# Optimization experiments

Measured on AMD Instinct MI355X. Metric: run time of the kernel, lower is better.

## Reference

```python
import jax, jax.numpy as jnp
import numpy as np

N, E, IN, H, OUT, G = 50000, 800000, 128, 256, 10, 512


def setup_inputs() -> dict:
    key = jax.random.key(0)
    ks = jax.random.split(key, 12)
    def lin(k, fan_in, fan_out):
        s = 1.0 / np.sqrt(fan_in)
        kw, kb = jax.random.split(k)
        W = jax.random.uniform(kw, (fan_in, fan_out), jnp.float32, -s, s)
        b = jax.random.uniform(kb, (fan_out,), jnp.float32, -s, s)
        return W, b
    x = jax.random.normal(ks[0], (N, IN), jnp.float32)
    edge_index = jax.random.randint(ks[1], (2, E), 0, N)
    batch = jnp.sort(jax.random.randint(ks[2], (N,), 0, G))
    W1a, b1a = lin(ks[3], IN, H)
    W1b, b1b = lin(ks[4], H, H)
    W2a, b2a = lin(ks[5], H, H)
    W2b, b2b = lin(ks[6], H, H)
    Wlin, blin = lin(ks[7], H, OUT)
    eps1 = jnp.zeros((), jnp.float32)
    eps2 = jnp.zeros((), jnp.float32)
    return dict(x=x, edge_index=edge_index, batch=batch,
                eps1=eps1, W1a=W1a, b1a=b1a, W1b=W1b, b1b=b1b,
                eps2=eps2, W2a=W2a, b2a=b2a, W2b=W2b, b2b=b2b,
                Wlin=Wlin, blin=blin)


def reference(x, edge_index, batch, eps1, W1a, b1a, W1b, b1b,
              eps2, W2a, b2a, W2b, b2b, Wlin, blin):
    src, dst = edge_index[0], edge_index[1]
    # GINConv 1: h = MLP((1+eps)*x + sum_{j in N(i)} x_j)
    agg = jax.ops.segment_sum(x[src], dst, num_segments=N)  # [N, IN]
    h = (1.0 + eps1) * x + agg
    h = jax.nn.relu(h @ W1a + b1a) @ W1b + b1b              # [N, H]
    h = jax.nn.relu(h)  # (dropout p=0.3 is identity in eval mode)
    # GINConv 2
    agg2 = jax.ops.segment_sum(h[src], dst, num_segments=N)  # [N, H]
    h2 = (1.0 + eps2) * h + agg2
    h2 = jax.nn.relu(h2 @ W2a + b2a) @ W2b + b2b             # [N, H]
    # global mean pool per graph
    psum = jax.ops.segment_sum(h2, batch, num_segments=G)    # [G, H]
    cnt = jax.ops.segment_sum(jnp.ones((N, 1), h2.dtype), batch, num_segments=G)
    pooled = psum / jnp.maximum(cnt, 1.0)
    out = pooled @ Wlin + blin                               # [G, OUT]
    return jax.nn.log_softmax(out, axis=-1)
```

## Files before the change

kernel.cpp:

```cpp
#include <hip/hip_runtime.h>
#include <math.h>
#include <stdint.h>

constexpr int N   = 50000;
constexpr int E   = 800000;
constexpr int IN  = 128;
constexpr int H   = 256;
constexpr int OUT = 10;
constexpr int G   = 512;
constexpr int BSTR = 64;

constexpr int NPART  = 391;
constexpr int SEGCAP = 48;
constexpr int EPB    = 4096;
constexpr int AB     = (E + EPB - 1) / EPB;

typedef __bf16 bf16x8 __attribute__((ext_vector_type(8)));
typedef float  f32x4  __attribute__((ext_vector_type(4)));
typedef float  f32x2  __attribute__((ext_vector_type(2)));

__device__ __forceinline__ float blo(unsigned v) { return __uint_as_float(v << 16); }
__device__ __forceinline__ float bhi(unsigned v) { return __uint_as_float(v & 0xffff0000u); }
__device__ __forceinline__ unsigned short f2b(float f) {
  unsigned u = __float_as_uint(f);
  u += 0x7fffu + ((u >> 16) & 1u);
  return (unsigned short)(u >> 16);
}
__device__ __forceinline__ unsigned packb(float lo, float hi) {
  return (unsigned)f2b(lo) | ((unsigned)f2b(hi) << 16);
}
__device__ __forceinline__ unsigned pk_fp8x4(float a, float b, float c, float d) {
  int r = 0;
  r = __builtin_amdgcn_cvt_pk_fp8_f32(a, b, r, false);
  r = __builtin_amdgcn_cvt_pk_fp8_f32(c, d, r, true);
  return (unsigned)r;
}
__device__ __forceinline__ unsigned char fp8_1(float v) {
  return (unsigned char)(__builtin_amdgcn_cvt_pk_fp8_f32(v, v, 0, false) & 0xff);
}

__device__ __forceinline__ void acc16(float* a, uint4 w, float s) {
  unsigned ws[4] = {w.x, w.y, w.z, w.w};
#pragma unroll
  for (int d = 0; d < 4; ++d) {
    f32x2 lo = __builtin_amdgcn_cvt_pk_f32_fp8((int)ws[d], false);
    f32x2 hi = __builtin_amdgcn_cvt_pk_f32_fp8((int)ws[d], true);
    a[4*d+0] = fmaf(s, lo.x, a[4*d+0]);
    a[4*d+1] = fmaf(s, lo.y, a[4*d+1]);
    a[4*d+2] = fmaf(s, hi.x, a[4*d+2]);
    a[4*d+3] = fmaf(s, hi.y, a[4*d+3]);
  }
}


constexpr int XQ_BLOCKS  = (N * IN / 4) / 256;
constexpr int W1A_BLOCKS = (256 * IN) / 256;
constexpr int WH_BLOCKS  = (256 * H) / 256;

__global__ __launch_bounds__(256) void prep_kernel(
    const int* __restrict__ srcp, const int* __restrict__ dstp,
    unsigned* __restrict__ pbuf, int* __restrict__ pcnt,
    const float* __restrict__ x, unsigned* __restrict__ xq,
    const float* __restrict__ W1a, unsigned short* __restrict__ Wt1a,
    const float* __restrict__ W1b, unsigned short* __restrict__ Wt1b,
    const float* __restrict__ W2a, unsigned short* __restrict__ Wt2a,
    const float* __restrict__ W2b, unsigned short* __restrict__ Wt2b) {
  __shared__ int lcur[NPART];
  int b = blockIdx.x;
  int t = threadIdx.x;
  if (b < AB) {
    for (int j = t; j < NPART; j += 256) lcur[j] = 0;
    __syncthreads();
    const int e0 = b * EPB;
#pragma unroll
    for (int r = 0; r < EPB / 1024; ++r) {
      int base = e0 + (r * 256 + t) * 4;
      if (base < E) {
        int4 d4 = *(const int4*)(dstp + base);
        int4 s4 = *(const int4*)(srcp + base);
        int dd[4] = {d4.x, d4.y, d4.z, d4.w};
        int ss[4] = {s4.x, s4.y, s4.z, s4.w};
#pragma unroll
        for (int u = 0; u < 4; ++u) {
          int part = dd[u] >> 7, dl = dd[u] & 127;
          int pos = atomicAdd(&lcur[part], 1);
          if (pos < SEGCAP)
            pbuf[((size_t)part * AB + b) * SEGCAP + pos] =
                ((unsigned)dl << 16) | (unsigned)ss[u];
        }
      }
    }
    __syncthreads();
    for (int j = t; j < NPART; j += 256) pcnt[b * NPART + j] = min(lcur[j], SEGCAP);
    return;
  }
  b -= AB;
  if (b < XQ_BLOCKS) {
    int id = b * 256 + t;
    float4 v = ((const float4*)x)[id];
    xq[id] = pk_fp8x4(v.x, v.y, v.z, v.w);
    return;
  }
  b -= XQ_BLOCKS;
  if (b < W1A_BLOCKS) {
    int id = b * 256 + t;
    int n = id >> 7, k = id & 127;
    Wt1a[id] = f2b(W1a[k * 256 + n]);
    return;
  }
  b -= W1A_BLOCKS;
  const float* Ws;
  unsigned short* Wd;
  if (b < WH_BLOCKS)            { Ws = W1b; Wd = Wt1b; }
  else if (b < 2 * WH_BLOCKS)   { Ws = W2a; Wd = Wt2a; b -= WH_BLOCKS; }
  else                          { Ws = W2b; Wd = Wt2b; b -= 2 * WH_BLOCKS; }
  int id = b * 256 + t;
  int n = id >> 8, k = id & 255;
  Wd[id] = f2b(Ws[k * 256 + n]);
}


__global__ __launch_bounds__(256) void csr_kernel(const unsigned* __restrict__ pbuf,
                                                  const int* __restrict__ pcnt,
                                                  int* __restrict__ deg, int* __restrict__ csre) {
  __shared__ int sa[256], sb[256];
  __shared__ int ldeg[128];
  int p = blockIdx.x;
  int t = threadIdx.x;
  if (t < 128) ldeg[t] = 0;
  sa[t] = (t < AB) ? pcnt[t * NPART + p] : 0;
  __syncthreads();
  int* cur = sa; int* nxt = sb;
#pragma unroll
  for (int off = 1; off < 256; off <<= 1) {
    nxt[t] = cur[t] + ((t >= off) ? cur[t - off] : 0);
    __syncthreads();
    int* tmp = cur; cur = nxt; nxt = tmp;
  }
  int T = cur[255];
  const unsigned* seg = pbuf + (size_t)p * AB * SEGCAP;
  for (int f = t; f < T; f += 256) {
    int lo = 0, hi = AB - 1;
    while (lo < hi) { int m = (lo + hi) >> 1; if (cur[m] > f) hi = m; else lo = m + 1; }
    int bb = lo;
    int excl = bb ? cur[bb - 1] : 0;
    unsigned v = seg[(size_t)bb * SEGCAP + (f - excl)];
    int dl = (int)(v >> 16), s = (int)(v & 0xFFFFu);
    int pos = atomicAdd(&ldeg[dl], 1);
    if (pos < BSTR) csre[(((size_t)p << 7) + dl) * BSTR + pos] = s;
  }
  __syncthreads();
  if (t < 128) {
    int node = (p << 7) + t;
    if (node < N) deg[node] = min(ldeg[t], BSTR);
  }
}


template <int K1, bool RELU2, bool OUT8>
__global__ __launch_bounds__(256, 2) void fused_mlp_kernel(
    const unsigned char* __restrict__ inq,
    const int* __restrict__ deg, const int* __restrict__ csre,
    const float* __restrict__ epsp,
    const unsigned short* __restrict__ Bta,
    const float* __restrict__ ba,
    const unsigned short* __restrict__ Btb,
    const float* __restrict__ bb,
    void* __restrict__ outv, int Nrows) {
  constexpr int LDK = 40, LDI = 168;
  constexpr int LDA = K1 + 40;
  constexpr int TPN = K1 / 32;
  constexpr int NPP = 256 / TPN;
  constexpr int PASSES = 64 / NPP;
  __shared__ __align__(16) unsigned short sh[10240 + 64 * LDA];
  unsigned short* Bs = sh;
  unsigned short* Af = sh + 10240;
  unsigned short* Is = sh + 10240;
  const int tid  = threadIdx.x;
  const int r0   = blockIdx.x * 64;
  const int wave = tid >> 6, lane = tid & 63;
  const int quad = lane >> 4, l15 = lane & 15;
  const int wrow = (wave >> 1) * 32, wcol = (wave & 1) * 64;
  const int srow = tid >> 2;
  const int sk8  = (tid & 3) * 8;

  {
    const float sc = 1.0f + epsp[0];
    const int slot = tid % TPN;
    const int nd0  = tid / TPN;
    const unsigned char* rb = inq + slot * 32;
#pragma unroll
    for (int ps = 0; ps < PASSES; ++ps) {
      const int node = ps * NPP + nd0;
      const int i = r0 + node;
      float a[32];
#pragma unroll
      for (int q = 0; q < 32; ++q) a[q] = 0.f;
      if (i < Nrows) {
        int dg = deg[i]; if (dg > BSTR) dg = BSTR;
        const int* bkt = csre + (size_t)i * BSTR;
        int j = 0;
        for (; j + 4 <= dg; j += 4) {
          uint4 v[8];
#pragma unroll
          for (int u = 0; u < 4; ++u) {
            unsigned raw = (unsigned)bkt[j + u];
            if (raw >= (unsigned)N) raw = 0u;
            const uint4* src = (const uint4*)(rb + (size_t)raw * K1);
            v[2*u]   = src[0];
            v[2*u+1] = src[1];
          }
#pragma unroll
          for (int u = 0; u < 4; ++u) {
            acc16(a,      v[2*u],   1.0f);
            acc16(a + 16, v[2*u+1], 1.0f);
          }
        }
        for (; j < dg; ++j) {
          unsigned raw = (unsigned)bkt[j];
          if (raw >= (unsigned)N) raw = 0u;
          const uint4* src = (const uint4*)(rb + (size_t)raw * K1);
          acc16(a, src[0], 1.0f);
          acc16(a + 16, src[1], 1.0f);
        }
        const uint4* sr = (const uint4*)(rb + (size_t)i * K1);
        acc16(a, sr[0], sc);
        acc16(a + 16, sr[1], sc);
      }
      uint4* dst = (uint4*)(Af + node * LDA + slot * 32);
#pragma unroll
      for (int w = 0; w < 4; ++w)
        dst[w] = make_uint4(packb(a[8*w+0], a[8*w+1]), packb(a[8*w+2], a[8*w+3]),
                            packb(a[8*w+4], a[8*w+5]), packb(a[8*w+6], a[8*w+7]));
    }
  }

  f32x4 acc1[2][2][4];
#pragma unroll
  for (int c = 0; c < 2; ++c)
#pragma unroll
    for (int i = 0; i < 2; ++i)
#pragma unroll
      for (int j = 0; j < 4; ++j) acc1[c][i][j] = (f32x4){0.f, 0.f, 0.f, 0.f};

  for (int k0 = 0; k0 < K1; k0 += 32) {
#pragma unroll
    for (int sgm = 0; sgm < 4; ++sgm) {
      int col = srow + sgm * 64;
      *(uint4*)(Bs + col * LDK + sk8) = *(const uint4*)(Bta + (size_t)col * K1 + k0 + sk8);
    }
    __syncthreads();
    bf16x8 af[2];
#pragma unroll
    for (int mt = 0; mt < 2; ++mt)
      af[mt] = *(const bf16x8*)(Af + (wrow + mt * 16 + l15) * LDA + k0 + quad * 8);
#pragma unroll
    for (int ch = 0; ch < 2; ++ch) {
      bf16x8 bfr[4];
#pragma unroll
      for (int nt = 0; nt < 4; ++nt)
        bfr[nt] = *(const bf16x8*)(Bs + (ch * 128 + wcol + nt * 16 + l15) * LDK + quad * 8);
#pragma unroll
      for (int mt = 0; mt < 2; ++mt)
#pragma unroll
        for (int nt = 0; nt < 4; ++nt)
          acc1[ch][mt][nt] =
              __builtin_amdgcn_mfma_f32_16x16x32_bf16(af[mt], bfr[nt], acc1[ch][mt][nt], 0, 0, 0);
    }
    __syncthreads();
  }

  float bva[2][4];
#pragma unroll
  for (int c = 0; c < 2; ++c)
#pragma unroll
    for (int nt = 0; nt < 4; ++nt) bva[c][nt] = ba[c * 128 + wcol + nt * 16 + l15];

  f32x4 acc2[2][2][4];
#pragma unroll
  for (int c = 0; c < 2; ++c)
#pragma unroll
    for (int i = 0; i < 2; ++i)
#pragma unroll
      for (int j = 0; j < 4; ++j) acc2[c][i][j] = (f32x4){0.f, 0.f, 0.f, 0.f};

  for (int ch = 0; ch < 2; ++ch) {
    __syncthreads();
#pragma unroll
    for (int mt = 0; mt < 2; ++mt)
#pragma unroll
      for (int nt = 0; nt < 4; ++nt) {
        int col = wcol + nt * 16 + l15;
        int rbase = wrow + mt * 16 + quad * 4;
#pragma unroll
        for (int i = 0; i < 4; ++i)
          Is[(rbase + i) * LDI + col] = f2b(fmaxf(acc1[ch][mt][nt][i] + bva[ch][nt], 0.f));
      }
    for (int kk = 0; kk < 4; ++kk) {
      __syncthreads();
      {
        int k0 = ch * 128 + kk * 32;
#pragma unroll
        for (int sgm = 0; sgm < 4; ++sgm) {
          int col = srow + sgm * 64;
          *(uint4*)(Bs + col * LDK + sk8) = *(const uint4*)(Btb + (size_t)col * 256 + k0 + sk8);
        }
      }
      __syncthreads();
      bf16x8 af[2];
#pragma unroll
      for (int mt = 0; mt < 2; ++mt)
        af[mt] = *(const bf16x8*)(Is + (wrow + mt * 16 + l15) * LDI + kk * 32 + quad * 8);
#pragma unroll
      for (int c2 = 0; c2 < 2; ++c2) {
        bf16x8 bfr[4];
#pragma unroll
        for (int nt = 0; nt < 4; ++nt)
          bfr[nt] = *(const bf16x8*)(Bs + (c2 * 128 + wcol + nt * 16 + l15) * LDK + quad * 8);
#pragma unroll
        for (int mt = 0; mt < 2; ++mt)
#pragma unroll
          for (int nt = 0; nt < 4; ++nt)
            acc2[c2][mt][nt] =
                __builtin_amdgcn_mfma_f32_16x16x32_bf16(af[mt], bfr[nt], acc2[c2][mt][nt], 0, 0, 0);
      }
    }
    __syncthreads();
  }

#pragma unroll
  for (int c2 = 0; c2 < 2; ++c2) {
    float bv[4];
#pragma unroll
    for (int nt = 0; nt < 4; ++nt) bv[nt] = bb[c2 * 128 + wcol + nt * 16 + l15];
#pragma unroll
    for (int mt = 0; mt < 2; ++mt) {
      int gr0 = r0 + wrow + mt * 16 + quad * 4;
#pragma unroll
      for (int i = 0; i < 4; ++i) {
        int grow = gr0 + i;
        if (grow >= Nrows) continue;
#pragma unroll
        for (int nt = 0; nt < 4; ++nt) {
          float v = acc2[c2][mt][nt][i] + bv[nt];
          if (RELU2) v = fmaxf(v, 0.f);
          int col = c2 * 128 + wcol + nt * 16 + l15;
          if (OUT8) ((unsigned char*)outv)[(size_t)grow * 256 + col] = fp8_1(v);
          else      ((unsigned short*)outv)[(size_t)grow * 256 + col] = f2b(v);
        }
      }
    }
  }
}


__global__ __launch_bounds__(128) void pool_final_kernel(const unsigned short* __restrict__ h2,
                                                         const int* __restrict__ batch,
                                                         const float* __restrict__ Wlin,
                                                         const float* __restrict__ blin,
                                                         float* __restrict__ out) {
  __shared__ float sp[H];
  __shared__ float logits[OUT];
  int g = blockIdx.x;
  int t = threadIdx.x;
  int lo = 0, hi = N;
  while (lo < hi) { int m = (lo + hi) >> 1; if (batch[m] < g) lo = m + 1; else hi = m; }
  int s = lo;
  lo = 0; hi = N;
  while (lo < hi) { int m = (lo + hi) >> 1; if (batch[m] < g + 1) lo = m + 1; else hi = m; }
  int e = lo;
  float a0 = 0.f, a1 = 0.f;
  const unsigned* base = (const unsigned*)h2;
  int n = s;
  for (; n + 4 <= e; n += 4) {
    unsigned v0 = base[(size_t)(n + 0) * (H / 2) + t];
    unsigned v1 = base[(size_t)(n + 1) * (H / 2) + t];
    unsigned v2 = base[(size_t)(n + 2) * (H / 2) + t];
    unsigned v3 = base[(size_t)(n + 3) * (H / 2) + t];
    a0 += blo(v0) + blo(v1) + blo(v2) + blo(v3);
    a1 += bhi(v0) + bhi(v1) + bhi(v2) + bhi(v3);
  }
  for (; n < e; ++n) {
    unsigned v = base[(size_t)n * (H / 2) + t];
    a0 += blo(v); a1 += bhi(v);
  }
  float inv = 1.0f / fmaxf((float)(e - s), 1.0f);
  sp[2 * t]     = a0 * inv;
  sp[2 * t + 1] = a1 * inv;
  __syncthreads();
  if (t < OUT) {
    float acc = blin[t];
    for (int k = 0; k < H; ++k) acc = fmaf(sp[k], Wlin[k * OUT + t], acc);
    logits[t] = acc;
  }
  __syncthreads();
  if (t == 0) {
    float m = -INFINITY;
    for (int j = 0; j < OUT; ++j) m = fmaxf(m, logits[j]);
    float ssum = 0.f;
    for (int j = 0; j < OUT; ++j) ssum += expf(logits[j] - m);
    float ls = logf(ssum);
    for (int j = 0; j < OUT; ++j) out[(size_t)g * OUT + j] = logits[j] - m - ls;
  }
}


static inline char* align_up(char* p, size_t a) {
  return (char*)(((uintptr_t)p + a - 1) & ~(a - 1));
}

extern "C" void kernel_launch(void* const* d_in, const int* in_sizes, int n_in,
                              void* d_out, int out_size, void* d_ws, size_t ws_size,
                              hipStream_t stream) {
  const float* x    = (const float*)d_in[0];
  const int*   ei   = (const int*)d_in[1];
  const int*   srcp = ei;
  const int*   dstp = ei + E;
  const int*   batch = (const int*)d_in[2];
  const float* eps1 = (const float*)d_in[3];
  const float* W1a  = (const float*)d_in[4];
  const float* b1a  = (const float*)d_in[5];
  const float* W1b  = (const float*)d_in[6];
  const float* b1b  = (const float*)d_in[7];
  const float* eps2 = (const float*)d_in[8];
  const float* W2a  = (const float*)d_in[9];
  const float* b2a  = (const float*)d_in[10];
  const float* W2b  = (const float*)d_in[11];
  const float* b2b  = (const float*)d_in[12];
  const float* Wlin = (const float*)d_in[13];
  const float* blin = (const float*)d_in[14];
  float* outp = (float*)d_out;

  char* p = (char*)d_ws;
  unsigned* pbuf = (unsigned*)p;     p = align_up(p + (size_t)NPART * AB * SEGCAP * 4, 256);
  int* pcnt = (int*)p;               p = align_up(p + (size_t)AB * NPART * 4, 256);
  int* deg  = (int*)p;               p = align_up(p + (size_t)N * 4, 256);
  int* csre = (int*)p;               p = align_up(p + (size_t)NPART * 128 * BSTR * 4, 256);
  unsigned* xq = (unsigned*)p;       p = align_up(p + (size_t)N * IN, 256);
  unsigned char* h1q = (unsigned char*)p;  p = align_up(p + (size_t)N * H, 256);
  unsigned short* B2 = (unsigned short*)p; p = align_up(p + (size_t)N * H * 2, 256);
  unsigned short* Wt1a = (unsigned short*)p;  p = align_up(p + (size_t)H * IN * 2, 256);
  unsigned short* Wt1b = (unsigned short*)p;  p = align_up(p + (size_t)H * H * 2, 256);
  unsigned short* Wt2a = (unsigned short*)p;  p = align_up(p + (size_t)H * H * 2, 256);
  unsigned short* Wt2b = (unsigned short*)p;  p = align_up(p + (size_t)H * H * 2, 256);

  prep_kernel<<<AB + XQ_BLOCKS + W1A_BLOCKS + 3 * WH_BLOCKS, 256, 0, stream>>>(
      srcp, dstp, pbuf, pcnt, x, xq, W1a, Wt1a, W1b, Wt1b, W2a, Wt2a, W2b, Wt2b);

  csr_kernel<<<NPART, 256, 0, stream>>>(pbuf, pcnt, deg, csre);

  const int nb = (N + 63) / 64;

  fused_mlp_kernel<IN, true, true><<<nb, 256, 0, stream>>>(
      (const unsigned char*)xq, deg, csre, eps1, Wt1a, b1a, Wt1b, b1b, h1q, N);

  fused_mlp_kernel<H, false, false><<<nb, 256, 0, stream>>>(
      h1q, deg, csre, eps2, Wt2a, b2a, Wt2b, b2b, B2, N);

  pool_final_kernel<<<G, 128, 0, stream>>>(B2, batch, Wlin, blin, outp);
}
```

Before: 258.3 us.

## Keep aggregated rows in registers and stage per-chunk to shrink LDS, raise occupancy

The aggregated input tile is no longer written whole into shared memory. Each thread keeps its packed bf16 rows in registers and writes only the current 32-wide K chunk into a small LDS buffer inside the GEMM loop. This shrinks the LDS footprint so launch bounds can ask for 3-4 blocks per CU, and the gather loop is unrolled to 8 neighbours to keep more loads in flight. The cost is higher register pressure from the pk array and the wider unroll, which could cause spills under the tighter occupancy bound.

Result: slower. 521.5 us (+101.9%).

```diff
diff --git a/kernel.cpp b/kernel.cpp
--- a/kernel.cpp
+++ b/kernel.cpp
@@ -158,7 +158,7 @@
 
 
 template <int K1, bool RELU2, bool OUT8>
-__global__ __launch_bounds__(256, 2) void fused_mlp_kernel(
+__global__ __launch_bounds__(256, (K1 == 128) ? 4 : 3) void fused_mlp_kernel(
     const unsigned char* __restrict__ inq,
     const int* __restrict__ deg, const int* __restrict__ csre,
     const float* __restrict__ epsp,
@@ -167,15 +167,15 @@
     const unsigned short* __restrict__ Btb,
     const float* __restrict__ bb,
     void* __restrict__ outv, int Nrows) {
-  constexpr int LDK = 40, LDI = 168;
-  constexpr int LDA = K1 + 40;
+  constexpr int LDK = 40, LDI = 136;
   constexpr int TPN = K1 / 32;
   constexpr int NPP = 256 / TPN;
   constexpr int PASSES = 64 / NPP;
-  __shared__ __align__(16) unsigned short sh[10240 + 64 * LDA];
-  unsigned short* Bs = sh;
-  unsigned short* Af = sh + 10240;
-  unsigned short* Is = sh + 10240;
+  constexpr int NCHUNK = K1 / 32;
+  __shared__ __align__(16) unsigned short sh[10240 + 64 * LDI];
+  unsigned short* Bs  = sh;
+  unsigned short* Afc = sh + 10240;
+  unsigned short* Is  = sh + 10240;
   const int tid  = threadIdx.x;
   const int r0   = blockIdx.x * 64;
   const int wave = tid >> 6, lane = tid & 63;
@@ -183,16 +183,16 @@
   const int wrow = (wave >> 1) * 32, wcol = (wave & 1) * 64;
   const int srow = tid >> 2;
   const int sk8  = (tid & 3) * 8;
-
+  const int slot = tid % TPN;
+  const int nd0  = tid / TPN;
+
+  uint4 pk[PASSES][4];
   {
     const float sc = 1.0f + epsp[0];
-    const int slot = tid % TPN;
-    const int nd0  = tid / TPN;
     const unsigned char* rb = inq + slot * 32;
 #pragma unroll
     for (int ps = 0; ps < PASSES; ++ps) {
-      const int node = ps * NPP + nd0;
-      const int i = r0 + node;
+      const int i = r0 + ps * NPP + nd0;
       float a[32];
 #pragma unroll
       for (int q = 0; q < 32; ++q) a[q] = 0.f;
@@ -200,13 +200,37 @@
         int dg = deg[i]; if (dg > BSTR) dg = BSTR;
         const int* bkt = csre + (size_t)i * BSTR;
         int j = 0;
+        for (; j + 8 <= dg; j += 8) {
+          unsigned idx[8];
+#pragma unroll
+          for (int u = 0; u < 8; ++u) {
+            unsigned raw = (unsigned)bkt[j + u];
+            idx[u] = raw < (unsigned)N ? raw : 0u;
+          }
+          uint4 v[16];
+#pragma unroll
+          for (int u = 0; u < 8; ++u) {
+            const uint4* src = (const uint4*)(rb + (size_t)idx[u] * K1);
+            v[2*u]   = src[0];
+            v[2*u+1] = src[1];
+          }
+#pragma unroll
+          for (int u = 0; u < 8; ++u) {
+            acc16(a,      v[2*u],   1.0f);
+            acc16(a + 16, v[2*u+1], 1.0f);
+          }
+        }
         for (; j + 4 <= dg; j += 4) {
-          uint4 v[8];
+          unsigned idx[4];
 #pragma unroll
           for (int u = 0; u < 4; ++u) {
             unsigned raw = (unsigned)bkt[j + u];
-            if (raw >= (unsigned)N) raw = 0u;
-            const uint4* src = (const uint4*)(rb + (size_t)raw * K1);
+            idx[u] = raw < (unsigned)N ? raw : 0u;
+          }
+          uint4 v[8];
+#pragma unroll
+          for (int u = 0; u < 4; ++u) {
+            const uint4* src = (const uint4*)(rb + (size_t)idx[u] * K1);
             v[2*u]   = src[0];
             v[2*u+1] = src[1];
           }
@@ -227,11 +251,10 @@
         acc16(a, sr[0], sc);
         acc16(a + 16, sr[1], sc);
       }
-      uint4* dst = (uint4*)(Af + node * LDA + slot * 32);
 #pragma unroll
       for (int w = 0; w < 4; ++w)
-        dst[w] = make_uint4(packb(a[8*w+0], a[8*w+1]), packb(a[8*w+2], a[8*w+3]),
-                            packb(a[8*w+4], a[8*w+5]), packb(a[8*w+6], a[8*w+7]));
+        pk[ps][w] = make_uint4(packb(a[8*w+0], a[8*w+1]), packb(a[8*w+2], a[8*w+3]),
+                               packb(a[8*w+4], a[8*w+5]), packb(a[8*w+6], a[8*w+7]));
     }
   }
 
@@ -243,17 +266,28 @@
 #pragma unroll
       for (int j = 0; j < 4; ++j) acc1[c][i][j] = (f32x4){0.f, 0.f, 0.f, 0.f};
 
-  for (int k0 = 0; k0 < K1; k0 += 32) {
+  for (int c = 0; c < NCHUNK; ++c) {
+    const int k0 = c * 32;
 #pragma unroll
     for (int sgm = 0; sgm < 4; ++sgm) {
       int col = srow + sgm * 64;
       *(uint4*)(Bs + col * LDK + sk8) = *(const uint4*)(Bta + (size_t)col * K1 + k0 + sk8);
     }
+    if (slot == c) {
+      uint4* d0 = (uint4*)(Afc + nd0 * LDK);
+#pragma unroll
+      for (int w = 0; w < 4; ++w) d0[w] = pk[0][w];
+      if constexpr (PASSES == 2) {
+        uint4* d1 = (uint4*)(Afc + (NPP + nd0) * LDK);
+#pragma unroll
+        for (int w = 0; w < 4; ++w) d1[w] = pk[1][w];
+      }
+    }
     __syncthreads();
     bf16x8 af[2];
 #pragma unroll
     for (int mt = 0; mt < 2; ++mt)
-      af[mt] = *(const bf16x8*)(Af + (wrow + mt * 16 + l15) * LDA + k0 + quad * 8);
+      af[mt] = *(const bf16x8*)(Afc + (wrow + mt * 16 + l15) * LDK + quad * 8);
 #pragma unroll
     for (int ch = 0; ch < 2; ++ch) {
       bf16x8 bfr[4];
```

## Halve fused MLP row tile to 32 and raise occupancy to four blocks

Applied to the files above, without the earlier changes.

The fused gather+MLP kernel now processes 32 nodes per block instead of 64, with each of the four waves owning 64 output columns over all 32 rows. The gather is restructured so 8 threads share one node and loads are batched per edge, and the second GEMM uses a full-width intermediate tile in a single K loop instead of two halves. Accumulator register count is halved and launch bounds request four blocks per CU, aiming to hide gather latency with more resident waves. The tradeoff is twice as many blocks, each reloading the full weight matrices through shared memory, which doubles weight traffic per row.

After: 330.1 us. 27.8% more time.

```diff
diff --git a/kernel.cpp b/kernel.cpp
--- a/kernel.cpp
+++ b/kernel.cpp
@@ -158,7 +158,7 @@
 
 
 template <int K1, bool RELU2, bool OUT8>
-__global__ __launch_bounds__(256, 2) void fused_mlp_kernel(
+__global__ __launch_bounds__(256, 4) void fused_mlp_kernel(
     const unsigned char* __restrict__ inq,
     const int* __restrict__ deg, const int* __restrict__ csre,
     const float* __restrict__ epsp,
@@ -167,81 +167,79 @@
     const unsigned short* __restrict__ Btb,
     const float* __restrict__ bb,
     void* __restrict__ outv, int Nrows) {
-  constexpr int LDK = 40, LDI = 168;
+  constexpr int LDK = 40;
   constexpr int LDA = K1 + 40;
-  constexpr int TPN = K1 / 32;
-  constexpr int NPP = 256 / TPN;
-  constexpr int PASSES = 64 / NPP;
-  __shared__ __align__(16) unsigned short sh[10240 + 64 * LDA];
+  constexpr int LDI = H + 40;
+  constexpr int W   = K1 / 8;
+  constexpr int LPN = W / 16;
+  constexpr int BATCH = 8 / LPN;
+  __shared__ __align__(16) unsigned short sh[10240 + 32 * LDI];
   unsigned short* Bs = sh;
   unsigned short* Af = sh + 10240;
   unsigned short* Is = sh + 10240;
   const int tid  = threadIdx.x;
-  const int r0   = blockIdx.x * 64;
+  const int r0   = blockIdx.x * 32;
   const int wave = tid >> 6, lane = tid & 63;
   const int quad = lane >> 4, l15 = lane & 15;
-  const int wrow = (wave >> 1) * 32, wcol = (wave & 1) * 64;
+  const int wcol = wave * 64;
   const int srow = tid >> 2;
   const int sk8  = (tid & 3) * 8;
 
   {
     const float sc = 1.0f + epsp[0];
-    const int slot = tid % TPN;
-    const int nd0  = tid / TPN;
-    const unsigned char* rb = inq + slot * 32;
-#pragma unroll
-    for (int ps = 0; ps < PASSES; ++ps) {
-      const int node = ps * NPP + nd0;
-      const int i = r0 + node;
-      float a[32];
-#pragma unroll
-      for (int q = 0; q < 32; ++q) a[q] = 0.f;
-      if (i < Nrows) {
-        int dg = deg[i]; if (dg > BSTR) dg = BSTR;
-        const int* bkt = csre + (size_t)i * BSTR;
-        int j = 0;
-        for (; j + 4 <= dg; j += 4) {
-          uint4 v[8];
-#pragma unroll
-          for (int u = 0; u < 4; ++u) {
-            unsigned raw = (unsigned)bkt[j + u];
-            if (raw >= (unsigned)N) raw = 0u;
-            const uint4* src = (const uint4*)(rb + (size_t)raw * K1);
-            v[2*u]   = src[0];
-            v[2*u+1] = src[1];
-          }
-#pragma unroll
-          for (int u = 0; u < 4; ++u) {
-            acc16(a,      v[2*u],   1.0f);
-            acc16(a + 16, v[2*u+1], 1.0f);
-          }
+    const int slot = tid & 7;
+    const int nd0  = tid >> 3;
+    const unsigned char* rb = inq + slot * W;
+    const int i = r0 + nd0;
+    float a[W];
+#pragma unroll
+    for (int q = 0; q < W; ++q) a[q] = 0.f;
+    if (i < Nrows) {
+      int dg = deg[i]; if (dg > BSTR) dg = BSTR;
+      const int* bkt = csre + (size_t)i * BSTR;
+      int j = 0;
+      for (; j + BATCH <= dg; j += BATCH) {
+        unsigned idx[BATCH];
+#pragma unroll
+        for (int u = 0; u < BATCH; ++u) {
+          unsigned raw = (unsigned)bkt[j + u];
+          idx[u] = raw < (unsigned)N ? raw : 0u;
         }
-        for (; j < dg; ++j) {
-          unsigned raw = (unsigned)bkt[j];
-          if (raw >= (unsigned)N) raw = 0u;
-          const uint4* src = (const uint4*)(rb + (size_t)raw * K1);
-          acc16(a, src[0], 1.0f);
-          acc16(a + 16, src[1], 1.0f);
+        uint4 v[8];
+#pragma unroll
+        for (int u = 0; u < BATCH; ++u) {
+          const uint4* src = (const uint4*)(rb + (size_t)idx[u] * K1);
+#pragma unroll
+          for (int p2 = 0; p2 < LPN; ++p2) v[u * LPN + p2] = src[p2];
         }
-        const uint4* sr = (const uint4*)(rb + (size_t)i * K1);
-        acc16(a, sr[0], sc);
-        acc16(a + 16, sr[1], sc);
+#pragma unroll
+        for (int u = 0; u < BATCH; ++u)
+#pragma unroll
+          for (int p2 = 0; p2 < LPN; ++p2) acc16(a + 16 * p2, v[u * LPN + p2], 1.0f);
       }
-      uint4* dst = (uint4*)(Af + node * LDA + slot * 32);
-#pragma unroll
-      for (int w = 0; w < 4; ++w)
-        dst[w] = make_uint4(packb(a[8*w+0], a[8*w+1]), packb(a[8*w+2], a[8*w+3]),
-                            packb(a[8*w+4], a[8*w+5]), packb(a[8*w+6], a[8*w+7]));
-    }
-  }
-
-  f32x4 acc1[2][2][4];
-#pragma unroll
-  for (int c = 0; c < 2; ++c)
-#pragma unroll
-    for (int i = 0; i < 2; ++i)
-#pragma unroll
-      for (int j = 0; j < 4; ++j) acc1[c][i][j] = (f32x4){0.f, 0.f, 0.f, 0.f};
+      for (; j < dg; ++j) {
+        unsigned raw = (unsigned)bkt[j];
+        if (raw >= (unsigned)N) raw = 0u;
+        const uint4* src = (const uint4*)(rb + (size_t)raw * K1);
+#pragma unroll
+        for (int p2 = 0; p2 < LPN; ++p2) acc16(a + 16 * p2, src[p2], 1.0f);
+      }
+      const uint4* sr = (const uint4*)(rb + (size_t)i * K1);
+#pragma unroll
+      for (int p2 = 0; p2 < LPN; ++p2) acc16(a + 16 * p2, sr[p2], sc);
+    }
+    uint4* dst = (uint4*)(Af + nd0 * LDA + slot * W);
+#pragma unroll
+    for (int w = 0; w < W / 8; ++w)
+      dst[w] = make_uint4(packb(a[8*w+0], a[8*w+1]), packb(a[8*w+2], a[8*w+3]),
+                          packb(a[8*w+4], a[8*w+5]), packb(a[8*w+6], a[8*w+7]));
+  }
+
+  f32x4 acc1[2][4];
+#pragma unroll
+  for (int i = 0; i < 2; ++i)
+#pragma unroll
+    for (int j = 0; j < 4; ++j) acc1[i][j] = (f32x4){0.f, 0.f, 0.f, 0.f};
 
   for (int k0 = 0; k0 < K1; k0 += 32) {
 #pragma unroll
@@ -253,101 +251,84 @@
     bf16x8 af[2];
 #pragma unroll
     for (int mt = 0; mt < 2; ++mt)
-      af[mt] = *(const bf16x8*)(Af + (wrow + mt * 16 + l15) * LDA + k0 + quad * 8);
-#pragma unroll
-    for (int ch = 0; ch < 2; ++ch) {
-      bf16x8 bfr[4];
+      af[mt] = *(const bf16x8*)(Af + (mt * 16 + l15) * LDA + k0 + quad * 8);
+    bf16x8 bfr[4];
+#pragma unroll
+    for (int nt = 0; nt < 4; ++nt)
+      bfr[nt] = *(const bf16x8*)(Bs + (wcol + nt * 16 + l15) * LDK + quad * 8);
+#pragma unroll
+    for (int mt = 0; mt < 2; ++mt)
 #pragma unroll
       for (int nt = 0; nt < 4; ++nt)
-        bfr[nt] = *(const bf16x8*)(Bs + (ch * 128 + wcol + nt * 16 + l15) * LDK + quad * 8);
-#pragma unroll
-      for (int mt = 0; mt < 2; ++mt)
-#pragma unroll
-        for (int nt = 0; nt < 4; ++nt)
-          acc1[ch][mt][nt] =
-              __builtin_amdgcn_mfma_f32_16x16x32_bf16(af[mt], bfr[nt], acc1[ch][mt][nt], 0, 0, 0);
-    }
-    __syncthreads();
-  }
-
-  float bva[2][4];
-#pragma unroll
-  for (int c = 0; c < 2; ++c)
-#pragma unroll
-    for (int nt = 0; nt < 4; ++nt) bva[c][nt] = ba[c * 128 + wcol + nt * 16 + l15];
-
-  f32x4 acc2[2][2][4];
-#pragma unroll
-  for (int c = 0; c < 2; ++c)
-#pragma unroll
-    for (int i = 0; i < 2; ++i)
-#pragma unroll
-      for (int j = 0; j < 4; ++j) acc2[c][i][j] = (f32x4){0.f, 0.f, 0.f, 0.f};
-
-  for (int ch = 0; ch < 2; ++ch) {
-    __syncthreads();
+        acc1[mt][nt] =
+            __builtin_amdgcn_mfma_f32_16x16x32_bf16(af[mt], bfr[nt], acc1[mt][nt], 0, 0, 0);
+    __syncthreads();
+  }
+
+  float bva[4];
+#pragma unroll
+  for (int nt = 0; nt < 4; ++nt) bva[nt] = ba[wcol + nt * 16 + l15];
+
+#pragma unroll
+  for (int mt = 0; mt < 2; ++mt)
+#pragma unroll
+    for (int nt = 0; nt < 4; ++nt) {
+      int col = wcol + nt * 16 + l15;
+      int rbase = mt * 16 + quad * 4;
+#pragma unroll
+      for (int i = 0; i < 4; ++i)
+        Is[(rbase + i) * LDI + col] = f2b(fmaxf(acc1[mt][nt][i] + bva[nt], 0.f));
+    }
+  __syncthreads();
+
+  f32x4 acc2[2][4];
+#pragma unroll
+  for (int i = 0; i < 2; ++i)
+#pragma unroll
+    for (int j = 0; j < 4; ++j) acc2[i][j] = (f32x4){0.f, 0.f, 0.f, 0.f};
+
+  for (int kk = 0; kk < H / 32; ++kk) {
+    const int k0 = kk * 32;
+#pragma unroll
+    for (int sgm = 0; sgm < 4; ++sgm) {
+      int col = srow + sgm * 64;
+      *(uint4*)(Bs + col * LDK + sk8) = *(const uint4*)(Btb + (size_t)col * 256 + k0 + sk8);
+    }
+    __syncthreads();
+    bf16x8 af[2];
 #pragma unroll
     for (int mt = 0; mt < 2; ++mt)
+      af[mt] = *(const bf16x8*)(Is + (mt * 16 + l15) * LDI + k0 + quad * 8);
+    bf16x8 bfr[4];
+#pragma unroll
+    for (int nt = 0; nt < 4; ++nt)
+      bfr[nt] = *(const bf16x8*)(Bs + (wcol + nt * 16 + l15) * LDK + quad * 8);
+#pragma unroll
+    for (int mt = 0; mt < 2; ++mt)
+#pragma unroll
+      for (int nt = 0; nt < 4; ++nt)
+        acc2[mt][nt] =
+            __builtin_amdgcn_mfma_f32_16x16x32_bf16(af[mt], bfr[nt], acc2[mt][nt], 0, 0, 0);
+    __syncthreads();
+  }
+
+  float bv[4];
+#pragma unroll
+  for (int nt = 0; nt < 4; ++nt) bv[nt] = bb[wcol + nt * 16 + l15];
+#pragma unroll
+  for (int mt = 0; mt < 2; ++mt) {
+    int gr0 = r0 + mt * 16 + quad * 4;
+#pragma unroll
+    for (int i = 0; i < 4; ++i) {
+      int grow = gr0 + i;
+      if (grow >= Nrows) continue;
 #pragma unroll
       for (int nt = 0; nt < 4; ++nt) {
+        float v = acc2[mt][nt][i] + bv[nt];
+        if (RELU2) v = fmaxf(v, 0.f);
         int col = wcol + nt * 16 + l15;
-        int rbase = wrow + mt * 16 + quad * 4;
-#pragma unroll
-        for (int i = 0; i < 4; ++i)
-          Is[(rbase + i) * LDI + col] = f2b(fmaxf(acc1[ch][mt][nt][i] + bva[ch][nt], 0.f));
-      }
-    for (int kk = 0; kk < 4; ++kk) {
-      __syncthreads();
-      {
-        int k0 = ch * 128 + kk * 32;
-#pragma unroll
-        for (int sgm = 0; sgm < 4; ++sgm) {
-          int col = srow + sgm * 64;
-          *(uint4*)(Bs + col * LDK + sk8) = *(const uint4*)(Btb + (size_t)col * 256 + k0 + sk8);
-        }
-      }
-      __syncthreads();
-      bf16x8 af[2];
-#pragma unroll
-      for (int mt = 0; mt < 2; ++mt)
-        af[mt] = *(const bf16x8*)(Is + (wrow + mt * 16 + l15) * LDI + kk * 32 + quad * 8);
-#pragma unroll
-      for (int c2 = 0; c2 < 2; ++c2) {
-        bf16x8 bfr[4];
-#pragma unroll
-        for (int nt = 0; nt < 4; ++nt)
-          bfr[nt] = *(const bf16x8*)(Bs + (c2 * 128 + wcol + nt * 16 + l15) * LDK + quad * 8);
-#pragma unroll
-        for (int mt = 0; mt < 2; ++mt)
-#pragma unroll
-          for (int nt = 0; nt < 4; ++nt)
-            acc2[c2][mt][nt] =
-                __builtin_amdgcn_mfma_f32_16x16x32_bf16(af[mt], bfr[nt], acc2[c2][mt][nt], 0, 0, 0);
-      }
-    }
-    __syncthreads();
-  }
-
-#pragma unroll
-  for (int c2 = 0; c2 < 2; ++c2) {
-    float bv[4];
-#pragma unroll
-    for (int nt = 0; nt < 4; ++nt) bv[nt] = bb[c2 * 128 + wcol + nt * 16 + l15];
-#pragma unroll
-    for (int mt = 0; mt < 2; ++mt) {
-      int gr0 = r0 + wrow + mt * 16 + quad * 4;
-#pragma unroll
-      for (int i = 0; i < 4; ++i) {
-        int grow = gr0 + i;
-        if (grow >= Nrows) continue;
-#pragma unroll
-        for (int nt = 0; nt < 4; ++nt) {
-          float v = acc2[c2][mt][nt][i] + bv[nt];
-          if (RELU2) v = fmaxf(v, 0.f);
-          int col = c2 * 128 + wcol + nt * 16 + l15;
-          if (OUT8) ((unsigned char*)outv)[(size_t)grow * 256 + col] = fp8_1(v);
-          else      ((unsigned short*)outv)[(size_t)grow * 256 + col] = f2b(v);
-        }
+        if (OUT8) ((unsigned char*)outv)[(size_t)grow * 256 + col] = fp8_1(v);
+        else      ((unsigned short*)outv)[(size_t)grow * 256 + col] = f2b(v);
       }
     }
   }
@@ -449,7 +430,7 @@
 
   csr_kernel<<<NPART, 256, 0, stream>>>(pbuf, pcnt, deg, csre);
 
-  const int nb = (N + 63) / 64;
+  const int nb = (N + 31) / 32;
 
   fused_mlp_kernel<IN, true, true><<<nb, 256, 0, stream>>>(
       (const unsigned char*)xq, deg, csre, eps1, Wt1a, b1a, Wt1b, b1b, h1q, N);
```
